# Kernel tuning notes

Measured on AMD Instinct MI355X. Metric: run time of the kernel, lower is better.

## Reference

```python
import jax, jax.numpy as jnp
import numpy as np

N = 100000   # nodes
R = 4        # relations
E = 200000   # edges per relation
IN = 256
HID = 64
OUT = 64
H = 8        # heads
NEG_SLOPE = 0.2


def setup_inputs() -> dict:
    key = jax.random.key(0)
    ks = jax.random.split(key, 13)
    s = 0.05
    return {
        "x": jax.random.normal(ks[0], (N, IN), jnp.float32),
        "src": jax.random.randint(ks[1], (R, E), 0, N),
        "dst": jax.random.randint(ks[2], (R, E), 0, N),
        "W0": jax.random.normal(ks[3], (R, IN, H * HID), jnp.float32) * s,
        "al0": jax.random.normal(ks[4], (R, H, HID), jnp.float32) * s,
        "ar0": jax.random.normal(ks[5], (R, H, HID), jnp.float32) * s,
        "W1": jax.random.normal(ks[6], (R, H * HID, H * HID), jnp.float32) * s,
        "al1": jax.random.normal(ks[7], (R, H, HID), jnp.float32) * s,
        "ar1": jax.random.normal(ks[8], (R, H, HID), jnp.float32) * s,
        "W2": jax.random.normal(ks[9], (R, H * HID, H * OUT), jnp.float32) * s,
        "al2": jax.random.normal(ks[10], (R, H, OUT), jnp.float32) * s,
        "ar2": jax.random.normal(ks[11], (R, H, OUT), jnp.float32) * s,
    }


def gat_layer(h, src, dst, W, al, ar):
    """Multi-relation GATConv layer; HeteroGraphConv sums ELU'd per-relation outputs.
    h: [N, in]; W: [R, in, H*O]; al/ar: [R, H, O]. Returns [N, H, O]."""
    n = h.shape[0]
    nheads, odim = al.shape[1], al.shape[2]
    acc = jnp.zeros((n, nheads, odim), h.dtype)
    for r in range(W.shape[0]):  # small fixed relation count
        f = (h @ W[r]).reshape(n, nheads, odim)          # [N,H,O]
        el = jnp.sum(f * al[r], axis=-1)                  # [N,H]
        er = jnp.sum(f * ar[r], axis=-1)                  # [N,H]
        s_r, d_r = src[r], dst[r]
        e = jax.nn.leaky_relu(el[s_r] + er[d_r], NEG_SLOPE)  # [E,H]
        # segment softmax over incoming edges per destination node
        m = jax.ops.segment_max(e, d_r, num_segments=n)
        m = jnp.where(jnp.isfinite(m), m, 0.0)
        ex = jnp.exp(e - m[d_r])
        denom = jax.ops.segment_sum(ex, d_r, num_segments=n)
        alpha = ex / (denom[d_r] + 1e-9)                  # [E,H]
        msg = f[s_r] * alpha[:, :, None]                  # [E,H,O]
        out_r = jax.ops.segment_sum(msg, d_r, num_segments=n)  # [N,H,O]
        acc = acc + jax.nn.elu(out_r)
    return acc


def reference(x, src, dst, W0, al0, ar0, W1, al1, ar1, W2, al2, ar2):
    h = gat_layer(x, src, dst, W0, al0, ar0).reshape(N, -1)   # flatten heads
    h = gat_layer(h, src, dst, W1, al1, ar1).reshape(N, -1)   # flatten heads
    h = gat_layer(h, src, dst, W2, al2, ar2).mean(axis=1)     # mean over heads
    return h
```

## Files before the change

### kernel.cpp

```cpp
#include <hip/hip_runtime.h>
#include <hip/hip_bf16.h>
#include <math.h>

#define NNODES 100000
#define NREL 4
#define NEDGE 200000
#define NH 8
#define FDIM 512
#define NMB 782

typedef float f4 __attribute__((ext_vector_type(4)));
typedef __bf16 bf16x8 __attribute__((ext_vector_type(8)));
typedef __bf16 bf16x4 __attribute__((ext_vector_type(4)));

__device__ __forceinline__ float eluf(float v) { return v > 0.f ? v : expm1f(v); }
__device__ __forceinline__ void gload16(const __bf16* g, __bf16* l) {
  __builtin_amdgcn_global_load_lds((const __attribute__((address_space(1))) void*)g,
                                   (__attribute__((address_space(3))) void*)l, 16, 0, 0);
}

__global__ void k_conv(const float* __restrict__ in, __bf16* __restrict__ outp) {
  int i = (blockIdx.x * 256 + threadIdx.x) * 4;
  f4 v = *(const f4*)(in + i);
  bf16x4 o = {(__bf16)v.x, (__bf16)v.y, (__bf16)v.z, (__bf16)v.w};
  *(bf16x4*)(outp + i) = o;
}

__global__ void k_transW(const float* __restrict__ W, __bf16* __restrict__ Wt, int K) {
  __shared__ float tile[32][33];
  int r = blockIdx.z;
  const float* Wr = W + (size_t)r * K * FDIM;
  __bf16* Wtr = Wt + (size_t)r * FDIM * K;
  int k0 = blockIdx.x * 32, n0 = blockIdx.y * 32;
  int tx = threadIdx.x, ty = threadIdx.y;
  for (int i = ty; i < 32; i += 8)
    tile[i][tx] = Wr[(size_t)(k0 + i) * FDIM + n0 + tx];
  __syncthreads();
  for (int i = ty; i < 32; i += 8)
    Wtr[(size_t)(n0 + i) * K + k0 + tx] = (__bf16)tile[tx][i];
}

__global__ __launch_bounds__(256, 2) void k_gemm(const __bf16* __restrict__ A,
                                                 const __bf16* __restrict__ BT,
                                                 __bf16* __restrict__ C,
                                                 const float* __restrict__ al,
                                                 const float* __restrict__ ar,
                                                 float* __restrict__ el,
                                                 float* __restrict__ er, int M, int K,
                                                 int nnbsh) {
  __shared__ alignas(16) __bf16 lA[2][128 * 32];
  __shared__ alignas(16) __bf16 lB[2][256 * 32];
  int t = threadIdx.x, l = t & 63, w = t >> 6;
  int nwg = gridDim.x, q = nwg >> 3, r8 = nwg & 7;
  int x = blockIdx.x & 7, loc = blockIdx.x >> 3;
  int swz = (x < r8 ? x * (q + 1) : r8 * (q + 1) + (x - r8) * q) + loc;
  int nnbm = (1 << nnbsh) - 1;
  int m0 = (swz >> nnbsh) * 128, n0 = (swz & nnbm) * 256;
  int NDIM = 256 << nnbsh;
  int nh_tot = 4 << nnbsh;
  int wm = (w >> 1) * 64, wn = (w & 1) * 128;
  f4 acc[4][8] = {};

  const __bf16* pA[2];
  const __bf16* pB[4];
#pragma unroll
  for (int u = 0; u < 2; u++) {
    int s = t + u * 256;
    int row = m0 + (s >> 2); if (row >= M) row = M - 1;
    pA[u] = A + (size_t)row * K + (((s & 3) ^ ((s >> 2) & 3)) * 8);
  }
#pragma unroll
  for (int u = 0; u < 4; u++) {
    int s = t + u * 256;
    pB[u] = BT + (size_t)(n0 + (s >> 2)) * K + (((s & 3) ^ ((s >> 2) & 3)) * 8);
  }

#define STAGE(buf, kk)                                      \
  do {                                                      \
    gload16(pA[0] + (kk), &lA[buf][t * 8]);                 \
    gload16(pA[1] + (kk), &lA[buf][(t + 256) * 8]);         \
    gload16(pB[0] + (kk), &lB[buf][t * 8]);                 \
    gload16(pB[1] + (kk), &lB[buf][(t + 256) * 8]);         \
    gload16(pB[2] + (kk), &lB[buf][(t + 512) * 8]);         \
    gload16(pB[3] + (kk), &lB[buf][(t + 768) * 8]);         \
  } while (0)

  int nt = K >> 5;
  STAGE(0, 0);
  STAGE(1, 32);
  int segoff = ((l >> 4) ^ (l & 3)) * 8;
  int rofA = (wm + (l & 15)) * 32 + segoff;
  int rofB = (wn + (l & 15)) * 32 + segoff;
  for (int kt = 0; kt < nt; kt++) {
    int cur = kt & 1;
    if (kt + 1 < nt) asm volatile("s_waitcnt vmcnt(6)" ::: "memory");
    else             asm volatile("s_waitcnt vmcnt(0)" ::: "memory");
    __builtin_amdgcn_s_barrier();
    bf16x8 a[4], b[8];
#pragma unroll
    for (int i = 0; i < 4; i++) a[i] = *(const bf16x8*)(&lA[cur][rofA + i * 512]);
#pragma unroll
    for (int j = 0; j < 8; j++) b[j] = *(const bf16x8*)(&lB[cur][rofB + j * 512]);
    asm volatile("s_waitcnt lgkmcnt(0)" ::: "memory");
    __builtin_amdgcn_s_barrier();
    if (kt + 2 < nt) STAGE(cur, (kt + 2) * 32);
#pragma unroll
    for (int i = 0; i < 4; i++)
#pragma unroll
      for (int j = 0; j < 8; j++)
        acc[i][j] = __builtin_amdgcn_mfma_f32_16x16x32_bf16(a[i], b[j], acc[i][j], 0, 0, 0);
  }
#undef STAGE

  int cn = n0 + wn + (l & 15);
  int rbase = m0 + wm + (l >> 4) * 4;
#pragma unroll
  for (int i = 0; i < 4; i++)
#pragma unroll
    for (int q2 = 0; q2 < 4; q2++) {
      int row = rbase + i * 16 + q2;
      if (row < M) {
#pragma unroll
        for (int j = 0; j < 8; j++)
          C[(size_t)row * NDIM + cn + j * 16] = (__bf16)acc[i][j][q2];
      }
    }

  int hbase = (n0 + wn) >> 6;
  float av[8], bv[8];
#pragma unroll
  for (int j = 0; j < 8; j++) {
    int h = hbase + (j >> 2);
    av[j] = al[h * 64 + (j & 3) * 16 + (l & 15)];
    bv[j] = ar[h * 64 + (j & 3) * 16 + (l & 15)];
  }
#pragma unroll
  for (int i = 0; i < 4; i++)
#pragma unroll
    for (int q2 = 0; q2 < 4; q2++) {
#pragma unroll
      for (int half = 0; half < 2; half++) {
        float se = acc[i][half * 4 + 0][q2] * av[half * 4 + 0] +
                   acc[i][half * 4 + 1][q2] * av[half * 4 + 1] +
                   acc[i][half * 4 + 2][q2] * av[half * 4 + 2] +
                   acc[i][half * 4 + 3][q2] * av[half * 4 + 3];
        float sr = acc[i][half * 4 + 0][q2] * bv[half * 4 + 0] +
                   acc[i][half * 4 + 1][q2] * bv[half * 4 + 1] +
                   acc[i][half * 4 + 2][q2] * bv[half * 4 + 2] +
                   acc[i][half * 4 + 3][q2] * bv[half * 4 + 3];
        se += __shfl_xor(se, 1); se += __shfl_xor(se, 2);
        se += __shfl_xor(se, 4); se += __shfl_xor(se, 8);
        sr += __shfl_xor(sr, 1); sr += __shfl_xor(sr, 2);
        sr += __shfl_xor(sr, 4); sr += __shfl_xor(sr, 8);
        if ((l & 15) == 0) {
          int row = rbase + i * 16 + q2;
          if (row < M) {
            int h = hbase + half;
            el[row * nh_tot + h] = se;
            er[row * nh_tot + h] = sr;
          }
        }
      }
    }
}

__global__ void k_count(const int* __restrict__ dst, int* __restrict__ deg) {
  int e = blockIdx.x * 256 + threadIdx.x;
  int r = blockIdx.y;
  if (e < NEDGE) {
    int d = dst[(size_t)r * NEDGE + e];
    if ((unsigned)d < (unsigned)NNODES) atomicAdd(&deg[r * NNODES + d], 1);
  }
}

__global__ __launch_bounds__(256) void k_scan_a(const int* __restrict__ in, int* __restrict__ out,
                                                int* __restrict__ bsum, int n) {
  __shared__ int wsums[4];
  int t = threadIdx.x, lane = t & 63, w = t >> 6;
  int base = blockIdx.x * 1024 + t * 4;
  int v0 = base + 0 < n ? in[base + 0] : 0;
  int v1 = base + 1 < n ? in[base + 1] : 0;
  int v2 = base + 2 < n ? in[base + 2] : 0;
  int v3 = base + 3 < n ? in[base + 3] : 0;
  int tot = v0 + v1 + v2 + v3;
  int sc = tot;
#pragma unroll
  for (int off = 1; off < 64; off <<= 1) {
    int u = __shfl_up(sc, off);
    if (lane >= off) sc += u;
  }
  if (lane == 63) wsums[w] = sc;
  __syncthreads();
  int add = 0;
#pragma unroll
  for (int i = 0; i < 4; i++)
    if (i < w) add += wsums[i];
  int excl = add + sc - tot;
  if (base + 0 < n) out[base + 0] = excl;
  if (base + 1 < n) out[base + 1] = excl + v0;
  if (base + 2 < n) out[base + 2] = excl + v0 + v1;
  if (base + 3 < n) out[base + 3] = excl + v0 + v1 + v2;
  if (t == 255) bsum[blockIdx.x] = add + sc;
}

__global__ __launch_bounds__(256) void k_scan_b(int* __restrict__ bsum, int nb) {
  __shared__ int wsums[4];
  int t = threadIdx.x, lane = t & 63, w = t >> 6;
  int i0 = t * 2, i1 = t * 2 + 1;
  int v0 = i0 < nb ? bsum[i0] : 0;
  int v1 = i1 < nb ? bsum[i1] : 0;
  int tot = v0 + v1, sc = tot;
#pragma unroll
  for (int off = 1; off < 64; off <<= 1) {
    int u = __shfl_up(sc, off);
    if (lane >= off) sc += u;
  }
  if (lane == 63) wsums[w] = sc;
  __syncthreads();
  int add = 0;
#pragma unroll
  for (int i = 0; i < 4; i++)
    if (i < w) add += wsums[i];
  int excl = add + sc - tot;
  if (i0 < nb) bsum[i0] = excl;
  if (i1 < nb) bsum[i1] = excl + v0;
}

__global__ void k_scan_c(int* __restrict__ out, const int* __restrict__ bsum, int n) {
  int i = blockIdx.x * 256 + threadIdx.x;
  if (i < n) out[i] += bsum[i >> 10];
}

__global__ void k_scatter(const int* __restrict__ src, const int* __restrict__ dst,
                          const int* __restrict__ ptrf, int* __restrict__ cur,
                          int* __restrict__ csrc) {
  int e = blockIdx.x * 256 + threadIdx.x;
  int r = blockIdx.y;
  if (e >= NEDGE) return;
  int d = dst[(size_t)r * NEDGE + e];
  if ((unsigned)d >= (unsigned)NNODES) return;
  int slot = ptrf[r * NNODES + d] + atomicAdd(&cur[r * NNODES + d], 1);
  if ((unsigned)slot < (unsigned)(NREL * NEDGE))
    csrc[slot] = src[(size_t)r * NEDGE + e];
}

__global__ void k_agg(const __bf16* __restrict__ f, const float* __restrict__ el,
                      const float* __restrict__ er, const int* __restrict__ ptrf,
                      const int* __restrict__ deg, const int* __restrict__ csrc,
                      __bf16* __restrict__ accG, int fstride, int estride, int nrr) {
  int t = threadIdx.x;
  int l = t & 63;
  int d = blockIdx.x * 4 + (t >> 6);
  int h = l >> 3;
  float res[8] = {0.f, 0.f, 0.f, 0.f, 0.f, 0.f, 0.f, 0.f};
  bool touched = false;
  for (int rr = 0; rr < nrr; rr++) {
    int cnt = deg[rr * NNODES + d];
    if (cnt <= 0) continue;
    touched = true;
    int start = ptrf[rr * NNODES + d];
    if (start < 0) start = 0;
    if (start > NREL * NEDGE) start = NREL * NEDGE;
    if (cnt > NREL * NEDGE - start) cnt = NREL * NEDGE - start;
    int eoff = rr * NH + h;
    int coff = rr * FDIM + l * 8;
    float erh = er[d * estride + eoff];
    float a[8] = {0.f, 0.f, 0.f, 0.f, 0.f, 0.f, 0.f, 0.f};
    float den = 0.f;
    for (int j = 0; j < cnt; j++) {
      int s = csrc[start + j];
      if ((unsigned)s >= (unsigned)NNODES) s = 0;
      float e = el[s * estride + eoff] + erh;
      e = (e > 0.f) ? e : 0.2f * e;
      float ex = __expf(e);
      den += ex;
      bf16x8 fv = *(const bf16x8*)(f + (size_t)s * fstride + coff);
#pragma unroll
      for (int i = 0; i < 8; i++) a[i] += ex * (float)fv[i];
    }
    float inv = 1.f / (den + 1e-9f);
#pragma unroll
    for (int i = 0; i < 8; i++) res[i] += eluf(a[i] * inv);
  }
  if (!touched) return;
  __bf16* ap = accG + (size_t)d * FDIM + l * 8;
  bf16x8 cv = *(bf16x8*)ap;
  bf16x8 o;
#pragma unroll
  for (int i = 0; i < 8; i++) o[i] = (__bf16)((float)cv[i] + res[i]);
  *(bf16x8*)ap = o;
}

__global__ void k_mean(const __bf16* __restrict__ acc, float* __restrict__ out) {
  int t = blockIdx.x * 256 + threadIdx.x;
  int n = t >> 6, o = t & 63;
  const __bf16* ap = acc + (size_t)n * FDIM + o;
  float s = 0.f;
#pragma unroll
  for (int h = 0; h < 8; h++) s += (float)ap[h * 64];
  out[t] = s * 0.125f;
}

extern "C" void kernel_launch(void* const* d_in, const int* in_sizes, int n_in,
                              void* d_out, int out_size, void* d_ws, size_t ws_size,
                              hipStream_t stream) {
  const float* x = (const float*)d_in[0];
  const int* srcp = (const int*)d_in[1];
  const int* dstp = (const int*)d_in[2];
  const float* Wl[3]  = {(const float*)d_in[3], (const float*)d_in[6], (const float*)d_in[9]};
  const float* alp[3] = {(const float*)d_in[4], (const float*)d_in[7], (const float*)d_in[10]};
  const float* arl[3] = {(const float*)d_in[5], (const float*)d_in[8], (const float*)d_in[11]};
  float* out = (float*)d_out;
  (void)in_sizes; (void)n_in; (void)out_size;

  auto rup = [](size_t b) { return (b + 255) & ~(size_t)255; };
  size_t sz_buf  = rup((size_t)NNODES * FDIM * 2);
  size_t sz_Wt   = rup((size_t)NREL * FDIM * FDIM * 2);
  size_t sz_int  = rup((size_t)NREL * NNODES * 4);
  size_t sz_csrc = rup((size_t)NREL * NEDGE * 4);
  size_t fixed = 2 * sz_buf + sz_Wt + 3 * sz_int + sz_csrc + rup(4096);
  size_t need2 = fixed + rup((size_t)NNODES * 1024 * 2) + 2 * rup((size_t)NNODES * 16 * 4);
  size_t need1 = fixed + rup((size_t)NNODES * 512 * 2)  + 2 * rup((size_t)NNODES * 8 * 4);
  int nb;
  if (ws_size >= need2) nb = 2;
  else if (ws_size >= need1) nb = 1;
  else return;

  int NDIM = nb * FDIM;
  int nheads = nb * NH;
  int nnbsh = (nb == 2) ? 2 : 1;

  char* ws = (char*)d_ws;
  size_t off = 0;
  auto alloc = [&](size_t bytes) -> void* { void* p = ws + off; off += rup(bytes); return p; };
  __bf16* bufA = (__bf16*)alloc((size_t)NNODES * FDIM * 2);
  __bf16* bufB = (__bf16*)alloc((size_t)NNODES * FDIM * 2);
  __bf16* fbuf = (__bf16*)alloc((size_t)NNODES * NDIM * 2);
  float* el    = (float*)alloc((size_t)NNODES * nheads * 4);
  float* er    = (float*)alloc((size_t)NNODES * nheads * 4);
  __bf16* Wt   = (__bf16*)alloc((size_t)NREL * FDIM * FDIM * 2);
  int* deg  = (int*)alloc((size_t)NREL * NNODES * 4);
  int* ptrf = (int*)alloc((size_t)NREL * NNODES * 4);
  int* cur  = (int*)alloc((size_t)NREL * NNODES * 4);
  int* csrc = (int*)alloc((size_t)NREL * NEDGE * 4);
  int* bsum = (int*)alloc(4096);

  hipMemsetAsync(deg, 0, (size_t)NREL * NNODES * 4, stream);
  hipMemsetAsync(cur, 0, (size_t)NREL * NNODES * 4, stream);
  k_count<<<dim3((NEDGE + 255) / 256, NREL), 256, 0, stream>>>(dstp, deg);
  int ntot = NREL * NNODES;
  int nb1 = (ntot + 1023) / 1024;
  k_scan_a<<<nb1, 256, 0, stream>>>(deg, ptrf, bsum, ntot);
  k_scan_b<<<1, 256, 0, stream>>>(bsum, nb1);
  k_scan_c<<<(ntot + 255) / 256, 256, 0, stream>>>(ptrf, bsum, ntot);
  k_scatter<<<dim3((NEDGE + 255) / 256, NREL), 256, 0, stream>>>(srcp, dstp, ptrf, cur, csrc);

  k_conv<<<(NNODES * 256) / 1024, 256, 0, stream>>>(x, bufA);

  __bf16* inb = bufA;
  __bf16* outb = bufB;
  for (int L = 0; L < 3; L++) {
    int K = (L == 0) ? 256 : FDIM;
    k_transW<<<dim3(K / 32, 16, NREL), dim3(32, 8), 0, stream>>>(Wl[L], Wt, K);
    hipMemsetAsync(outb, 0, (size_t)NNODES * FDIM * 2, stream);
    int ngrid = NMB * (NDIM / 256);
    for (int g = 0; g < NREL / nb; g++) {
      k_gemm<<<ngrid, 256, 0, stream>>>(inb, Wt + (size_t)g * nb * FDIM * K, fbuf,
                                        alp[L] + (size_t)g * nb * 512,
                                        arl[L] + (size_t)g * nb * 512,
                                        el, er, NNODES, K, nnbsh);
      k_agg<<<NNODES / 4, 256, 0, stream>>>(fbuf, el, er, ptrf + (size_t)g * nb * NNODES,
                                            deg + (size_t)g * nb * NNODES, csrc, outb,
                                            NDIM, nheads, nb);
    }
    __bf16* tmp = inb; inb = outb; outb = tmp;
  }
  k_mean<<<(NNODES * 64) / 256, 256, 0, stream>>>(inb, out);
}
```

Baseline: 2.210 ms.

## Process one relation per GEMM, stage GEMM output through LDS, drop memset

Removes the two-relations-per-pass path so each relation runs its own GEMM and aggregation, with the first relation's aggregation writing the output directly instead of relying on a memset and a read-modify-write. The GEMM epilogue now stages the accumulator tile through a swizzled LDS region and issues 16-byte coalesced row stores instead of scattered 2-byte stores. The occupancy hint in launch bounds is dropped. This trades more kernel launches and smaller per-launch grids for cheaper stores, a smaller working set and no zero-fill pass.

```diff
diff --git a/kernel.cpp b/kernel.cpp
--- a/kernel.cpp
+++ b/kernel.cpp
@@ -40,24 +40,20 @@
     Wtr[(size_t)(n0 + i) * K + k0 + tx] = (__bf16)tile[tx][i];
 }
 
-__global__ __launch_bounds__(256, 2) void k_gemm(const __bf16* __restrict__ A,
-                                                 const __bf16* __restrict__ BT,
-                                                 __bf16* __restrict__ C,
-                                                 const float* __restrict__ al,
-                                                 const float* __restrict__ ar,
-                                                 float* __restrict__ el,
-                                                 float* __restrict__ er, int M, int K,
-                                                 int nnbsh) {
+__global__ __launch_bounds__(256) void k_gemm(const __bf16* __restrict__ A,
+                                              const __bf16* __restrict__ BT,
+                                              __bf16* __restrict__ C,
+                                              const float* __restrict__ al,
+                                              const float* __restrict__ ar,
+                                              float* __restrict__ el,
+                                              float* __restrict__ er, int M, int K) {
   __shared__ alignas(16) __bf16 lA[2][128 * 32];
   __shared__ alignas(16) __bf16 lB[2][256 * 32];
   int t = threadIdx.x, l = t & 63, w = t >> 6;
-  int nwg = gridDim.x, q = nwg >> 3, r8 = nwg & 7;
-  int x = blockIdx.x & 7, loc = blockIdx.x >> 3;
-  int swz = (x < r8 ? x * (q + 1) : r8 * (q + 1) + (x - r8) * q) + loc;
-  int nnbm = (1 << nnbsh) - 1;
-  int m0 = (swz >> nnbsh) * 128, n0 = (swz & nnbm) * 256;
-  int NDIM = 256 << nnbsh;
-  int nh_tot = 4 << nnbsh;
+  int nwg = gridDim.x, q8 = nwg >> 3, r8 = nwg & 7;
+  int xx = blockIdx.x & 7, loc = blockIdx.x >> 3;
+  int swz = (xx < r8 ? xx * (q8 + 1) : r8 * (q8 + 1) + (xx - r8) * q8) + loc;
+  int m0 = (swz >> 1) * 128, n0 = (swz & 1) * 256;
   int wm = (w >> 1) * 64, wn = (w & 1) * 128;
   f4 acc[4][8] = {};
 
@@ -112,56 +108,74 @@
   }
 #undef STAGE
 
-  int cn = n0 + wn + (l & 15);
+  int hbase = (n0 + wn) >> 6;
   int rbase = m0 + wm + (l >> 4) * 4;
-#pragma unroll
-  for (int i = 0; i < 4; i++)
-#pragma unroll
-    for (int q2 = 0; q2 < 4; q2++) {
-      int row = rbase + i * 16 + q2;
-      if (row < M) {
-#pragma unroll
-        for (int j = 0; j < 8; j++)
-          C[(size_t)row * NDIM + cn + j * 16] = (__bf16)acc[i][j][q2];
-      }
-    }
-
-  int hbase = (n0 + wn) >> 6;
-  float av[8], bv[8];
-#pragma unroll
-  for (int j = 0; j < 8; j++) {
-    int h = hbase + (j >> 2);
-    av[j] = al[h * 64 + (j & 3) * 16 + (l & 15)];
-    bv[j] = ar[h * 64 + (j & 3) * 16 + (l & 15)];
-  }
-#pragma unroll
-  for (int i = 0; i < 4; i++)
-#pragma unroll
-    for (int q2 = 0; q2 < 4; q2++) {
-#pragma unroll
-      for (int half = 0; half < 2; half++) {
-        float se = acc[i][half * 4 + 0][q2] * av[half * 4 + 0] +
-                   acc[i][half * 4 + 1][q2] * av[half * 4 + 1] +
-                   acc[i][half * 4 + 2][q2] * av[half * 4 + 2] +
-                   acc[i][half * 4 + 3][q2] * av[half * 4 + 3];
-        float sr = acc[i][half * 4 + 0][q2] * bv[half * 4 + 0] +
-                   acc[i][half * 4 + 1][q2] * bv[half * 4 + 1] +
-                   acc[i][half * 4 + 2][q2] * bv[half * 4 + 2] +
-                   acc[i][half * 4 + 3][q2] * bv[half * 4 + 3];
-        se += __shfl_xor(se, 1); se += __shfl_xor(se, 2);
-        se += __shfl_xor(se, 4); se += __shfl_xor(se, 8);
-        sr += __shfl_xor(sr, 1); sr += __shfl_xor(sr, 2);
-        sr += __shfl_xor(sr, 4); sr += __shfl_xor(sr, 8);
-        if ((l & 15) == 0) {
-          int row = rbase + i * 16 + q2;
-          if (row < M) {
-            int h = hbase + half;
-            el[row * nh_tot + h] = se;
-            er[row * nh_tot + h] = sr;
+  {
+    float av[8], bv[8];
+#pragma unroll
+    for (int j = 0; j < 8; j++) {
+      int h = hbase + (j >> 2);
+      av[j] = al[h * 64 + (j & 3) * 16 + (l & 15)];
+      bv[j] = ar[h * 64 + (j & 3) * 16 + (l & 15)];
+    }
+#pragma unroll
+    for (int i = 0; i < 4; i++)
+#pragma unroll
+      for (int q2 = 0; q2 < 4; q2++) {
+#pragma unroll
+        for (int half = 0; half < 2; half++) {
+          float se = acc[i][half * 4 + 0][q2] * av[half * 4 + 0] +
+                     acc[i][half * 4 + 1][q2] * av[half * 4 + 1] +
+                     acc[i][half * 4 + 2][q2] * av[half * 4 + 2] +
+                     acc[i][half * 4 + 3][q2] * av[half * 4 + 3];
+          float sr = acc[i][half * 4 + 0][q2] * bv[half * 4 + 0] +
+                     acc[i][half * 4 + 1][q2] * bv[half * 4 + 1] +
+                     acc[i][half * 4 + 2][q2] * bv[half * 4 + 2] +
+                     acc[i][half * 4 + 3][q2] * bv[half * 4 + 3];
+          se += __shfl_xor(se, 1); se += __shfl_xor(se, 2);
+          se += __shfl_xor(se, 4); se += __shfl_xor(se, 8);
+          sr += __shfl_xor(sr, 1); sr += __shfl_xor(sr, 2);
+          sr += __shfl_xor(sr, 4); sr += __shfl_xor(sr, 8);
+          if ((l & 15) == 0) {
+            int row = rbase + i * 16 + q2;
+            if (row < M) {
+              int h = hbase + half;
+              el[row * NH + h] = se;
+              er[row * NH + h] = sr;
+            }
           }
         }
       }
-    }
+  }
+
+  __bf16* rep = &lB[0][0] + w * 2048;
+#pragma unroll
+  for (int i = 0; i < 4; i++) {
+#pragma unroll
+    for (int q2 = 0; q2 < 4; q2++) {
+      int rr = (l >> 4) * 4 + q2;
+      int sw_hi = ((rr >> 2) & 3) << 1;
+#pragma unroll
+      for (int j = 0; j < 8; j++) {
+        int col = (l & 15) + j * 16;
+        int c8 = (col >> 3) ^ sw_hi;
+        rep[rr * 128 + c8 * 8 + (col & 7)] = (__bf16)acc[i][j][q2];
+      }
+    }
+    asm volatile("s_waitcnt lgkmcnt(0)" ::: "memory");
+    __builtin_amdgcn_sched_barrier(0);
+#pragma unroll
+    for (int tt = 0; tt < 4; tt++) {
+      int rr = tt * 4 + (l >> 4);
+      int c8 = (l & 15) ^ (((rr >> 2) & 3) << 1);
+      bf16x8 v = *(const bf16x8*)(rep + rr * 128 + c8 * 8);
+      int grow = m0 + wm + i * 16 + rr;
+      if (grow < M)
+        *(bf16x8*)(&C[(size_t)grow * FDIM + n0 + wn + (l & 15) * 8]) = v;
+    }
+    asm volatile("s_waitcnt lgkmcnt(0)" ::: "memory");
+    __builtin_amdgcn_sched_barrier(0);
+  }
 }
 
 __global__ void k_count(const int* __restrict__ dst, int* __restrict__ deg) {
@@ -247,47 +261,48 @@
 __global__ void k_agg(const __bf16* __restrict__ f, const float* __restrict__ el,
                       const float* __restrict__ er, const int* __restrict__ ptrf,
                       const int* __restrict__ deg, const int* __restrict__ csrc,
-                      __bf16* __restrict__ accG, int fstride, int estride, int nrr) {
+                      __bf16* __restrict__ accG, int writeMode) {
   int t = threadIdx.x;
   int l = t & 63;
   int d = blockIdx.x * 4 + (t >> 6);
   int h = l >> 3;
+  int cnt = deg[d];
   float res[8] = {0.f, 0.f, 0.f, 0.f, 0.f, 0.f, 0.f, 0.f};
-  bool touched = false;
-  for (int rr = 0; rr < nrr; rr++) {
-    int cnt = deg[rr * NNODES + d];
-    if (cnt <= 0) continue;
-    touched = true;
-    int start = ptrf[rr * NNODES + d];
+  if (cnt > 0) {
+    int start = ptrf[d];
     if (start < 0) start = 0;
     if (start > NREL * NEDGE) start = NREL * NEDGE;
     if (cnt > NREL * NEDGE - start) cnt = NREL * NEDGE - start;
-    int eoff = rr * NH + h;
-    int coff = rr * FDIM + l * 8;
-    float erh = er[d * estride + eoff];
+    float erh = er[d * NH + h];
     float a[8] = {0.f, 0.f, 0.f, 0.f, 0.f, 0.f, 0.f, 0.f};
     float den = 0.f;
     for (int j = 0; j < cnt; j++) {
       int s = csrc[start + j];
       if ((unsigned)s >= (unsigned)NNODES) s = 0;
-      float e = el[s * estride + eoff] + erh;
+      float e = el[s * NH + h] + erh;
       e = (e > 0.f) ? e : 0.2f * e;
       float ex = __expf(e);
       den += ex;
-      bf16x8 fv = *(const bf16x8*)(f + (size_t)s * fstride + coff);
+      bf16x8 fv = *(const bf16x8*)(f + (size_t)s * FDIM + l * 8);
 #pragma unroll
       for (int i = 0; i < 8; i++) a[i] += ex * (float)fv[i];
     }
     float inv = 1.f / (den + 1e-9f);
 #pragma unroll
-    for (int i = 0; i < 8; i++) res[i] += eluf(a[i] * inv);
-  }
-  if (!touched) return;
+    for (int i = 0; i < 8; i++) res[i] = eluf(a[i] * inv);
+  } else if (!writeMode) {
+    return;
+  }
   __bf16* ap = accG + (size_t)d * FDIM + l * 8;
-  bf16x8 cv = *(bf16x8*)ap;
   bf16x8 o;
-#pragma unroll
-  for (int i = 0; i < 8; i++) o[i] = (__bf16)((float)cv[i] + res[i]);
+  if (writeMode) {
+#pragma unroll
+    for (int i = 0; i < 8; i++) o[i] = (__bf16)res[i];
+  } else {
+    bf16x8 cv = *(bf16x8*)ap;
+#pragma unroll
+    for (int i = 0; i < 8; i++) o[i] = (__bf16)((float)cv[i] + res[i]);
+  }
   *(bf16x8*)ap = o;
 }
 
@@ -314,30 +329,21 @@
   (void)in_sizes; (void)n_in; (void)out_size;
 
   auto rup = [](size_t b) { return (b + 255) & ~(size_t)255; };
-  size_t sz_buf  = rup((size_t)NNODES * FDIM * 2);
-  size_t sz_Wt   = rup((size_t)NREL * FDIM * FDIM * 2);
-  size_t sz_int  = rup((size_t)NREL * NNODES * 4);
-  size_t sz_csrc = rup((size_t)NREL * NEDGE * 4);
-  size_t fixed = 2 * sz_buf + sz_Wt + 3 * sz_int + sz_csrc + rup(4096);
-  size_t need2 = fixed + rup((size_t)NNODES * 1024 * 2) + 2 * rup((size_t)NNODES * 16 * 4);
-  size_t need1 = fixed + rup((size_t)NNODES * 512 * 2)  + 2 * rup((size_t)NNODES * 8 * 4);
-  int nb;
-  if (ws_size >= need2) nb = 2;
-  else if (ws_size >= need1) nb = 1;
-  else return;
-
-  int NDIM = nb * FDIM;
-  int nheads = nb * NH;
-  int nnbsh = (nb == 2) ? 2 : 1;
+  size_t need = 3 * rup((size_t)NNODES * FDIM * 2) +
+                2 * rup((size_t)NNODES * NH * 4) +
+                rup((size_t)NREL * FDIM * FDIM * 2) +
+                3 * rup((size_t)NREL * NNODES * 4) +
+                rup((size_t)NREL * NEDGE * 4) + rup(4096);
+  if (ws_size < need) return;
 
   char* ws = (char*)d_ws;
   size_t off = 0;
   auto alloc = [&](size_t bytes) -> void* { void* p = ws + off; off += rup(bytes); return p; };
   __bf16* bufA = (__bf16*)alloc((size_t)NNODES * FDIM * 2);
   __bf16* bufB = (__bf16*)alloc((size_t)NNODES * FDIM * 2);
-  __bf16* fbuf = (__bf16*)alloc((size_t)NNODES * NDIM * 2);
-  float* el    = (float*)alloc((size_t)NNODES * nheads * 4);
-  float* er    = (float*)alloc((size_t)NNODES * nheads * 4);
+  __bf16* fbuf = (__bf16*)alloc((size_t)NNODES * FDIM * 2);
+  float* el    = (float*)alloc((size_t)NNODES * NH * 4);
+  float* er    = (float*)alloc((size_t)NNODES * NH * 4);
   __bf16* Wt   = (__bf16*)alloc((size_t)NREL * FDIM * FDIM * 2);
   int* deg  = (int*)alloc((size_t)NREL * NNODES * 4);
   int* ptrf = (int*)alloc((size_t)NREL * NNODES * 4);
@@ -359,19 +365,18 @@
 
   __bf16* inb = bufA;
   __bf16* outb = bufB;
+  int ngrid = NMB * 2;
   for (int L = 0; L < 3; L++) {
     int K = (L == 0) ? 256 : FDIM;
     k_transW<<<dim3(K / 32, 16, NREL), dim3(32, 8), 0, stream>>>(Wl[L], Wt, K);
-    hipMemsetAsync(outb, 0, (size_t)NNODES * FDIM * 2, stream);
-    int ngrid = NMB * (NDIM / 256);
-    for (int g = 0; g < NREL / nb; g++) {
-      k_gemm<<<ngrid, 256, 0, stream>>>(inb, Wt + (size_t)g * nb * FDIM * K, fbuf,
-                                        alp[L] + (size_t)g * nb * 512,
-                                        arl[L] + (size_t)g * nb * 512,
-                                        el, er, NNODES, K, nnbsh);
-      k_agg<<<NNODES / 4, 256, 0, stream>>>(fbuf, el, er, ptrf + (size_t)g * nb * NNODES,
-                                            deg + (size_t)g * nb * NNODES, csrc, outb,
-                                            NDIM, nheads, nb);
+    for (int r = 0; r < NREL; r++) {
+      k_gemm<<<ngrid, 256, 0, stream>>>(inb, Wt + (size_t)r * FDIM * K, fbuf,
+                                        alp[L] + (size_t)r * 512,
+                                        arl[L] + (size_t)r * 512,
+                                        el, er, NNODES, K);
+      k_agg<<<NNODES / 4, 256, 0, stream>>>(fbuf, el, er, ptrf + (size_t)r * NNODES,
+                                            deg + (size_t)r * NNODES, csrc, outb,
+                                            r == 0 ? 1 : 0);
     }
     __bf16* tmp = inb; inb = outb; outb = tmp;
   }
```

Result: slower. 2.735 ms (+23.8%).
